# Optimization experiments

Hardware: AMD Instinct MI355X
Metric: run time of the kernel (lower is better)

The kernel has to match this reference:

```python
import jax, jax.numpy as jnp
import numpy as np

N, F, H = 512, 256, 512

def _w(k, i, o):
    return jax.random.normal(k, (i, o), jnp.float32) * (1.0 / np.sqrt(i))

def setup_inputs() -> dict:
    key = jax.random.key(0)
    ks = jax.random.split(key, 12)
    z = lambda n: jnp.zeros((n,), jnp.float32)
    return {
        "node_features": jax.random.normal(ks[0], (N, F), jnp.float32),
        "adjacency": jax.random.uniform(ks[1], (N, N), jnp.float32),
        # GraphConv layers: neighbor linear (wl,bl) and self-loop (ws,bs)
        "gc1_wl": _w(ks[2], F, H), "gc1_bl": z(H), "gc1_ws": _w(ks[3], F, H), "gc1_bs": z(H),
        "gc2_wl": _w(ks[4], H, H), "gc2_bl": z(H), "gc2_ws": _w(ks[5], H, H), "gc2_bs": z(H),
        "gc3_wl": _w(ks[6], H, F), "gc3_bl": z(F), "gc3_ws": _w(ks[7], H, F), "gc3_bs": z(F),
        # edge MLP: Linear(2F,H) -> ReLU -> (dropout=identity, eval) -> Linear(H,H) -> ReLU -> Linear(H,1)
        "mlp_w1": _w(ks[8], 2 * F, H), "mlp_b1": z(H),
        "mlp_w2": _w(ks[9], H, H), "mlp_b2": z(H),
        "mlp_w3": _w(ks[10], H, 1), "mlp_b3": z(1),
    }

def _gconv(x, adj_norm, wl, bl, ws, bs):
    # adj_norm @ Linear(x) + SelfLoop(x)
    return adj_norm @ (x @ wl + bl) + (x @ ws + bs)

def reference(node_features, adjacency,
              gc1_wl, gc1_bl, gc1_ws, gc1_bs,
              gc2_wl, gc2_bl, gc2_ws, gc2_bs,
              gc3_wl, gc3_bl, gc3_ws, gc3_bs,
              mlp_w1, mlp_b1, mlp_w2, mlp_b2, mlp_w3, mlp_b3):
    # row-normalized adjacency (shared across all three layers)
    adj_norm = adjacency / (adjacency.sum(axis=1, keepdims=True) + 1e-8)
    x = jax.nn.relu(_gconv(node_features, adj_norm, gc1_wl, gc1_bl, gc1_ws, gc1_bs))
    x = jax.nn.relu(_gconv(x, adj_norm, gc2_wl, gc2_bl, gc2_ws, gc2_bs))
    emb = _gconv(x, adj_norm, gc3_wl, gc3_bl, gc3_ws, gc3_bs)  # [N, F]
    # vectorized all-pairs (i<j) edge scoring, symmetric scatter
    iu, ju = np.triu_indices(N, k=1)  # static index lists, P = N(N-1)/2
    ef = jnp.concatenate([emb[iu], emb[ju]], axis=-1)  # [P, 2F]
    h = jax.nn.relu(ef @ mlp_w1 + mlp_b1)
    h = jax.nn.relu(h @ mlp_w2 + mlp_b2)
    s = jax.nn.sigmoid((h @ mlp_w3 + mlp_b3)[:, 0])  # [P]
    edge_scores = jnp.zeros((N, N), emb.dtype).at[iu, ju].set(s).at[ju, iu].set(s)
    return emb, edge_scores
```

## Files before the change

kernel.cpp:

```cpp
#include <hip/hip_runtime.h>
#include <hip/hip_bf16.h>


#define NN 512
#define FF 256
#define HH 512

typedef __attribute__((ext_vector_type(8))) short s8v;
typedef __attribute__((ext_vector_type(4))) float f4v;

__device__ __forceinline__ ushort f2bf(float f) {
  unsigned u = __float_as_uint(f);
  unsigned r = (u + 0x7fffu + ((u >> 16) & 1u)) >> 16;
  return (ushort)r;
}

__global__ __launch_bounds__(256)
void rownorm_kernel(const float* __restrict__ adj, float* __restrict__ adjn) {
  int row = blockIdx.x;
  int tid = threadIdx.x;
  const float* r = adj + row * NN;
  float a0 = r[tid], a1 = r[tid + 256];
  float s = a0 + a1;
#pragma unroll
  for (int m = 1; m < 64; m <<= 1) s += __shfl_xor(s, m);
  __shared__ float wsum[4];
  if ((tid & 63) == 0) wsum[tid >> 6] = s;
  __syncthreads();
  float inv = 1.f / (wsum[0] + wsum[1] + wsum[2] + wsum[3] + 1e-8f);
  float* o = adjn + row * NN;
  o[tid] = a0 * inv;
  o[tid + 256] = a1 * inv;
}

template <bool RELU>
__global__ __launch_bounds__(256)
void gemm_ts(int M, int N, int K,
             const float* __restrict__ A, int lda,
             const float* __restrict__ B0, const float* __restrict__ B1, int ldb,
             const float* __restrict__ bias0, const float* __restrict__ bias1,
             const float* __restrict__ add0, const float* __restrict__ add1, int ldadd,
             float* __restrict__ C0, float* __restrict__ C1, int ldc)
{
  const float* B = blockIdx.z ? B1 : B0;
  const float* bias = blockIdx.z ? bias1 : bias0;
  const float* add = blockIdx.z ? add1 : add0;
  float* C = blockIdx.z ? C1 : C0;
  const int n0 = blockIdx.x * 64;
  const int m0 = blockIdx.y * 16;
  const int tid = threadIdx.x;
  const int ty = tid >> 4, tx = tid & 15;

  __shared__ float As[32][18];
  __shared__ float Bs[32][68];
  float4 acc = {0.f, 0.f, 0.f, 0.f};

  const int am = tid >> 4;
  const int ak = tid & 15;
  const int bk = tid >> 4;
  const int bn = tid & 15;

  float2 pa = *(const float2*)&A[(m0 + am) * lda + ak * 2];
  float4 pb0 = *(const float4*)&B[bk * ldb + n0 + bn * 4];
  float4 pb1 = *(const float4*)&B[(bk + 16) * ldb + n0 + bn * 4];

  for (int k0 = 0; k0 < K; k0 += 32) {
    As[ak * 2][am] = pa.x;
    As[ak * 2 + 1][am] = pa.y;
    *(float4*)&Bs[bk][bn * 4] = pb0;
    *(float4*)&Bs[bk + 16][bn * 4] = pb1;
    __syncthreads();
    if (k0 + 32 < K) {
      pa = *(const float2*)&A[(m0 + am) * lda + k0 + 32 + ak * 2];
      pb0 = *(const float4*)&B[(k0 + 32 + bk) * ldb + n0 + bn * 4];
      pb1 = *(const float4*)&B[(k0 + 48 + bk) * ldb + n0 + bn * 4];
    }
#pragma unroll
    for (int k = 0; k < 32; ++k) {
      float a = As[k][ty];
      float4 b = *(const float4*)&Bs[k][tx * 4];
      acc.x += a * b.x; acc.y += a * b.y; acc.z += a * b.z; acc.w += a * b.w;
    }
    __syncthreads();
  }

  int m = m0 + ty;
  float4 v = acc;
  if (bias) {
    float4 bv = *(const float4*)&bias[n0 + tx * 4];
    v.x += bv.x; v.y += bv.y; v.z += bv.z; v.w += bv.w;
  }
  if (add) {
    float4 d = *(const float4*)&add[m * ldadd + n0 + tx * 4];
    v.x += d.x; v.y += d.y; v.z += d.z; v.w += d.w;
  }
  if (RELU) {
    v.x = fmaxf(v.x, 0.f); v.y = fmaxf(v.y, 0.f);
    v.z = fmaxf(v.z, 0.f); v.w = fmaxf(v.w, 0.f);
  }
  *(float4*)&C[m * ldc + n0 + tx * 4] = v;
}

__global__ __launch_bounds__(256)
void w2_pack(const float* __restrict__ w2, ushort* __restrict__ w2t2) {
  int slab = blockIdx.y;
  int col = blockIdx.x * 64 + (threadIdx.x >> 2);
  int kq = threadIdx.x & 3;
  int k0 = slab * 32 + kq * 8;
  ushort tmp[8];
#pragma unroll
  for (int e = 0; e < 8; ++e) tmp[e] = f2bf(w2[(k0 + e) * HH + col]);
  ushort* dst = w2t2 + slab * 16384 + col * 32 + kq * 8;
  *(ushort4*)dst = *(ushort4*)tmp;
  *(ushort4*)(dst + 4) = *(ushort4*)&tmp[4];
}

__global__ __launch_bounds__(512)
__attribute__((amdgpu_waves_per_eu(2, 2)))
void edge_mlp(const float* __restrict__ Amat, const float* __restrict__ Bmat,
              const ushort* __restrict__ w2t2,
              const float* __restrict__ b2, const float* __restrict__ w3,
              const float* __restrict__ b3,
              float* __restrict__ edges)
{
  __shared__ ushort h1s[2][128 * 128];
  __shared__ float part[8][640];

  const int tb = (int)blockIdx.x;
  int bj = (int)((sqrtf(4.f * tb + 1.f) - 1.f) * 0.5f);
  while (bj * bj + bj > tb) --bj;
  while ((bj + 1) * (bj + 2) <= tb) ++bj;
  const int bi = tb - bj * bj - bj;

  const int tid = threadIdx.x;
  const int wid = tid >> 6;
  const int lane = tid & 63;
  const int l15 = lane & 15;
  const int lg = lane >> 4;

  const f4v zero = {0.f, 0.f, 0.f, 0.f};
  f4v acc[8][4];
#pragma unroll
  for (int mf = 0; mf < 8; ++mf)
#pragma unroll
    for (int nf = 0; nf < 4; ++nf) acc[mf][nf] = zero;

  float4 sa[4], sb[4];
  auto issue_half = [&](int ch, int h) {
#pragma unroll
    for (int q = 0; q < 4; ++q) {
      int fidx = (h * 4 + q) * 512 + tid;
      int p = fidx >> 5;
      int k4 = fidx & 31;
      int i = bi * 8 + (p >> 4);
      int j = bj * 16 + (p & 15);
      sa[q] = *(const float4*)(Amat + i * HH + ch * 128 + k4 * 4);
      sb[q] = *(const float4*)(Bmat + j * HH + ch * 128 + k4 * 4);
    }
  };
  auto write_half = [&](int buf, int h) {
#pragma unroll
    for (int q = 0; q < 4; ++q) {
      int fidx = (h * 4 + q) * 512 + tid;
      int p = fidx >> 5;
      int k4 = fidx & 31;
      ushort4 pk;
      pk.x = f2bf(fmaxf(sa[q].x + sb[q].x, 0.f));
      pk.y = f2bf(fmaxf(sa[q].y + sb[q].y, 0.f));
      pk.z = f2bf(fmaxf(sa[q].z + sb[q].z, 0.f));
      pk.w = f2bf(fmaxf(sa[q].w + sb[q].w, 0.f));
      int off = (p * 256 + k4 * 8) ^ ((p & 7) << 4);
      *(ushort4*)((char*)h1s[buf] + off) = pk;
    }
  };

  issue_half(0, 0); write_half(0, 0);
  issue_half(0, 1); write_half(0, 1);
  __syncthreads();

  const ushort* wbase = w2t2 + wid * 2048 + l15 * 32 + lg * 8;

  s8v nb0, nb1, nb2, nb3;
  nb0 = *(const s8v*)wbase;
  nb1 = *(const s8v*)(wbase + 512);
  nb2 = *(const s8v*)(wbase + 1024);
  nb3 = *(const s8v*)(wbase + 1536);

  auto slab_step = [&](int cur, int slab) {
    s8v cb0 = nb0, cb1 = nb1, cb2 = nb2, cb3 = nb3;
    if (slab < 15) {
      const ushort* wb = wbase + (slab + 1) * 16384;
      nb0 = *(const s8v*)wb;
      nb1 = *(const s8v*)(wb + 512);
      nb2 = *(const s8v*)(wb + 1024);
      nb3 = *(const s8v*)(wb + 1536);
    }
    int ks = slab & 3;
#pragma unroll
    for (int mf = 0; mf < 8; ++mf) {
      int p = mf * 16 + l15;
      int off = (p * 256 + ks * 64 + lg * 16) ^ ((p & 7) << 4);
      s8v a = *(const s8v*)((const char*)h1s[cur] + off);
      acc[mf][0] = __builtin_amdgcn_mfma_f32_16x16x32_bf16(a, cb0, acc[mf][0], 0, 0, 0);
      acc[mf][1] = __builtin_amdgcn_mfma_f32_16x16x32_bf16(a, cb1, acc[mf][1], 0, 0, 0);
      acc[mf][2] = __builtin_amdgcn_mfma_f32_16x16x32_bf16(a, cb2, acc[mf][2], 0, 0, 0);
      acc[mf][3] = __builtin_amdgcn_mfma_f32_16x16x32_bf16(a, cb3, acc[mf][3], 0, 0, 0);
    }
  };

  for (int ch = 0; ch < 4; ++ch) {
    int cur = ch & 1;
    if (ch < 3) issue_half(ch + 1, 0);
    slab_step(cur, ch * 4 + 0);
    slab_step(cur, ch * 4 + 1);
    if (ch < 3) {
      write_half(cur ^ 1, 0);
      issue_half(ch + 1, 1);
    }
    slab_step(cur, ch * 4 + 2);
    slab_step(cur, ch * 4 + 3);
    if (ch < 3) write_half(cur ^ 1, 1);
    __syncthreads();
  }

  float bb[4], ww[4];
#pragma unroll
  for (int nf = 0; nf < 4; ++nf) {
    int col = wid * 64 + nf * 16 + l15;
    bb[nf] = b2[col];
    ww[nf] = w3[col];
  }
#pragma unroll
  for (int mf = 0; mf < 8; ++mf) {
    float ps[4];
#pragma unroll
    for (int e = 0; e < 4; ++e) {
      ps[e] = fmaxf(acc[mf][0][e] + bb[0], 0.f) * ww[0] +
              fmaxf(acc[mf][1][e] + bb[1], 0.f) * ww[1] +
              fmaxf(acc[mf][2][e] + bb[2], 0.f) * ww[2] +
              fmaxf(acc[mf][3][e] + bb[3], 0.f) * ww[3];
    }
#pragma unroll
    for (int m = 1; m < 16; m <<= 1) {
#pragma unroll
      for (int e = 0; e < 4; ++e) ps[e] += __shfl_xor(ps[e], m);
    }
    if (l15 == 0) {
#pragma unroll
      for (int e = 0; e < 4; ++e)
        part[wid][mf * 16 + lg * 4 + e] = ps[e];
    }
  }
  __syncthreads();
  if (tid < 128) {
    float tot = b3[0];
#pragma unroll
    for (int w = 0; w < 8; ++w) tot += part[w][tid];
    float sg = 1.f / (1.f + expf(-tot));
    int i = bi * 8 + (tid >> 4);
    int j = bj * 16 + (tid & 15);
    if (i < j) {
      edges[i * NN + j] = sg;
      edges[j * NN + i] = sg;
    } else if (i == j) {
      edges[i * NN + i] = 0.f;
    }
  }
}

extern "C" void kernel_launch(void* const* d_in, const int* in_sizes, int n_in,
                              void* d_out, int out_size, void* d_ws, size_t ws_size,
                              hipStream_t stream) {
  const float* node = (const float*)d_in[0];
  const float* adj  = (const float*)d_in[1];
  const float* g1wl = (const float*)d_in[2];
  const float* g1bl = (const float*)d_in[3];
  const float* g1ws = (const float*)d_in[4];
  const float* g1bs = (const float*)d_in[5];
  const float* g2wl = (const float*)d_in[6];
  const float* g2bl = (const float*)d_in[7];
  const float* g2ws = (const float*)d_in[8];
  const float* g2bs = (const float*)d_in[9];
  const float* g3wl = (const float*)d_in[10];
  const float* g3bl = (const float*)d_in[11];
  const float* g3ws = (const float*)d_in[12];
  const float* g3bs = (const float*)d_in[13];
  const float* w1 = (const float*)d_in[14];
  const float* b1 = (const float*)d_in[15];
  const float* w2 = (const float*)d_in[16];
  const float* b2 = (const float*)d_in[17];
  const float* w3 = (const float*)d_in[18];
  const float* b3 = (const float*)d_in[19];

  float* out = (float*)d_out;
  float* emb = out;
  float* edges = out + NN * FF;

  char* wsb = (char*)d_ws;
  float* adjn = (float*)wsb;
  float* Tb   = (float*)(wsb + (1u << 20));
  float* Sb   = (float*)(wsb + (2u << 20));
  float* xa   = (float*)(wsb + (3u << 20));
  float* xb   = (float*)(wsb + (4u << 20));
  ushort* w2t2 = (ushort*)(wsb + (5u << 20));
  float* Amat = Tb;
  float* Bmat = Sb;

  rownorm_kernel<<<NN, 256, 0, stream>>>(adj, adjn);
  w2_pack<<<dim3(8, 16), 256, 0, stream>>>(w2, w2t2);

  gemm_ts<false><<<dim3(8, 32, 2), 256, 0, stream>>>(
      NN, HH, FF, node, FF, g1wl, g1ws, HH, g1bl, g1bs,
      nullptr, nullptr, 0, Tb, Sb, HH);
  gemm_ts<true><<<dim3(8, 32, 1), 256, 0, stream>>>(
      NN, HH, NN, adjn, NN, Tb, Tb, HH, nullptr, nullptr,
      Sb, Sb, HH, xa, xa, HH);
  gemm_ts<false><<<dim3(8, 32, 2), 256, 0, stream>>>(
      NN, HH, HH, xa, HH, g2wl, g2ws, HH, g2bl, g2bs,
      nullptr, nullptr, 0, Tb, Sb, HH);
  gemm_ts<true><<<dim3(8, 32, 1), 256, 0, stream>>>(
      NN, HH, NN, adjn, NN, Tb, Tb, HH, nullptr, nullptr,
      Sb, Sb, HH, xb, xb, HH);
  gemm_ts<false><<<dim3(4, 32, 2), 256, 0, stream>>>(
      NN, FF, HH, xb, HH, g3wl, g3ws, FF, g3bl, g3bs,
      nullptr, nullptr, 0, Tb, Sb, FF);
  gemm_ts<false><<<dim3(4, 32, 1), 256, 0, stream>>>(
      NN, FF, NN, adjn, NN, Tb, Tb, FF, nullptr, nullptr,
      Sb, Sb, FF, emb, emb, FF);

  gemm_ts<false><<<dim3(8, 32, 2), 256, 0, stream>>>(
      NN, HH, FF, emb, FF, w1, w1 + FF * HH, HH, b1, nullptr,
      nullptr, nullptr, 0, Amat, Bmat, HH);

  edge_mlp<<<1056, 512, 0, stream>>>(Amat, Bmat, w2t2, b2, w3, b3, edges);
}
```

Baseline: 194.3 us.

## Merge prep kernels, halve GEMM row tile, raise MFMA wave priority

Folds the adjacency row-normalisation and the W2 bf16 packing into one launch, which removes a kernel launch. The small fp32 GEMMs drop from 16 to 8 rows per block, doubling the grid to fill more compute units, at the cost of less B-tile reuse per block. The edge MLP raises wave priority around its MFMA loop with s_setprio so matrix work is issued ahead of the other waves' loads.

```diff
diff --git a/kernel.cpp b/kernel.cpp
--- a/kernel.cpp
+++ b/kernel.cpp
@@ -16,103 +16,104 @@
 }
 
 __global__ __launch_bounds__(256)
-void rownorm_kernel(const float* __restrict__ adj, float* __restrict__ adjn) {
-  int row = blockIdx.x;
+void prep_kernel(const float* __restrict__ adj, float* __restrict__ adjn,
+                 const float* __restrict__ w2, ushort* __restrict__ w2t2) {
+  int b = blockIdx.x;
   int tid = threadIdx.x;
-  const float* r = adj + row * NN;
-  float a0 = r[tid], a1 = r[tid + 256];
-  float s = a0 + a1;
-#pragma unroll
-  for (int m = 1; m < 64; m <<= 1) s += __shfl_xor(s, m);
-  __shared__ float wsum[4];
-  if ((tid & 63) == 0) wsum[tid >> 6] = s;
-  __syncthreads();
-  float inv = 1.f / (wsum[0] + wsum[1] + wsum[2] + wsum[3] + 1e-8f);
-  float* o = adjn + row * NN;
-  o[tid] = a0 * inv;
-  o[tid + 256] = a1 * inv;
+  if (b < 512) {
+    const float* r = adj + b * NN;
+    float a0 = r[tid], a1 = r[tid + 256];
+    float s = a0 + a1;
+#pragma unroll
+    for (int m = 1; m < 64; m <<= 1) s += __shfl_xor(s, m);
+    __shared__ float wsum[4];
+    if ((tid & 63) == 0) wsum[tid >> 6] = s;
+    __syncthreads();
+    float inv = 1.f / (wsum[0] + wsum[1] + wsum[2] + wsum[3] + 1e-8f);
+    float* o = adjn + b * NN;
+    o[tid] = a0 * inv;
+    o[tid + 256] = a1 * inv;
+  } else {
+    int b2 = b - 512;
+    int slab = b2 >> 3;
+    int col = (b2 & 7) * 64 + (tid >> 2);
+    int kq = tid & 3;
+    int k0 = slab * 32 + kq * 8;
+    ushort tmp[8];
+#pragma unroll
+    for (int e = 0; e < 8; ++e) tmp[e] = f2bf(w2[(k0 + e) * HH + col]);
+    ushort* dst = w2t2 + slab * 16384 + col * 32 + kq * 8;
+    *(ushort4*)dst = *(ushort4*)tmp;
+    *(ushort4*)(dst + 4) = *(ushort4*)&tmp[4];
+  }
 }
 
 template <bool RELU>
 __global__ __launch_bounds__(256)
-void gemm_ts(int M, int N, int K,
-             const float* __restrict__ A, int lda,
-             const float* __restrict__ B0, const float* __restrict__ B1, int ldb,
-             const float* __restrict__ bias0, const float* __restrict__ bias1,
-             const float* __restrict__ add0, const float* __restrict__ add1, int ldadd,
-             float* __restrict__ C0, float* __restrict__ C1, int ldc)
+void gemm_ts8(int K,
+              const float* __restrict__ A, int lda,
+              const float* __restrict__ B0, const float* __restrict__ B1, int ldb,
+              const float* __restrict__ bias0, const float* __restrict__ bias1,
+              const float* __restrict__ add0, const float* __restrict__ add1, int ldadd,
+              float* __restrict__ C0, float* __restrict__ C1, int ldc)
 {
   const float* B = blockIdx.z ? B1 : B0;
   const float* bias = blockIdx.z ? bias1 : bias0;
   const float* add = blockIdx.z ? add1 : add0;
   float* C = blockIdx.z ? C1 : C0;
   const int n0 = blockIdx.x * 64;
-  const int m0 = blockIdx.y * 16;
+  const int m0 = blockIdx.y * 8;
   const int tid = threadIdx.x;
-  const int ty = tid >> 4, tx = tid & 15;
-
-  __shared__ float As[32][18];
-  __shared__ float Bs[32][68];
-  float4 acc = {0.f, 0.f, 0.f, 0.f};
-
-  const int am = tid >> 4;
-  const int ak = tid & 15;
-  const int bk = tid >> 4;
-  const int bn = tid & 15;
-
-  float2 pa = *(const float2*)&A[(m0 + am) * lda + ak * 2];
-  float4 pb0 = *(const float4*)&B[bk * ldb + n0 + bn * 4];
-  float4 pb1 = *(const float4*)&B[(bk + 16) * ldb + n0 + bn * 4];
+  const int row = tid >> 5;
+  const int cp = tid & 31;
+
+  __shared__ float As[32][9];
+  __shared__ float Bs[32][66];
+  float2 acc = {0.f, 0.f};
+
+  const int am = tid >> 5, ak = tid & 31;
+  const int br = tid >> 3, bc = (tid & 7) * 4;
+
+  float pa = A[(m0 + am) * lda + ak];
+  float4 pb0 = *(const float4*)&B[br * ldb + n0 + bc];
+  float4 pb1 = *(const float4*)&B[br * ldb + n0 + 32 + bc];
 
   for (int k0 = 0; k0 < K; k0 += 32) {
-    As[ak * 2][am] = pa.x;
-    As[ak * 2 + 1][am] = pa.y;
-    *(float4*)&Bs[bk][bn * 4] = pb0;
-    *(float4*)&Bs[bk + 16][bn * 4] = pb1;
+    As[ak][am] = pa;
+    *(float4*)&Bs[br][bc] = pb0;
+    *(float4*)&Bs[br][32 + bc] = pb1;
     __syncthreads();
     if (k0 + 32 < K) {
-      pa = *(const float2*)&A[(m0 + am) * lda + k0 + 32 + ak * 2];
-      pb0 = *(const float4*)&B[(k0 + 32 + bk) * ldb + n0 + bn * 4];
-      pb1 = *(const float4*)&B[(k0 + 48 + bk) * ldb + n0 + bn * 4];
+      pa = A[(m0 + am) * lda + k0 + 32 + ak];
+      pb0 = *(const float4*)&B[(k0 + 32 + br) * ldb + n0 + bc];
+      pb1 = *(const float4*)&B[(k0 + 32 + br) * ldb + n0 + 32 + bc];
     }
 #pragma unroll
     for (int k = 0; k < 32; ++k) {
-      float a = As[k][ty];
-      float4 b = *(const float4*)&Bs[k][tx * 4];
-      acc.x += a * b.x; acc.y += a * b.y; acc.z += a * b.z; acc.w += a * b.w;
+      float a = As[k][row];
+      float2 b = *(const float2*)&Bs[k][cp * 2];
+      acc.x += a * b.x;
+      acc.y += a * b.y;
     }
     __syncthreads();
   }
 
-  int m = m0 + ty;
-  float4 v = acc;
+  int m = m0 + row;
+  int col = n0 + cp * 2;
+  float2 v = acc;
   if (bias) {
-    float4 bv = *(const float4*)&bias[n0 + tx * 4];
-    v.x += bv.x; v.y += bv.y; v.z += bv.z; v.w += bv.w;
+    float2 bv = *(const float2*)&bias[col];
+    v.x += bv.x; v.y += bv.y;
   }
   if (add) {
-    float4 d = *(const float4*)&add[m * ldadd + n0 + tx * 4];
-    v.x += d.x; v.y += d.y; v.z += d.z; v.w += d.w;
+    float2 d = *(const float2*)&add[m * ldadd + col];
+    v.x += d.x; v.y += d.y;
   }
   if (RELU) {
-    v.x = fmaxf(v.x, 0.f); v.y = fmaxf(v.y, 0.f);
-    v.z = fmaxf(v.z, 0.f); v.w = fmaxf(v.w, 0.f);
-  }
-  *(float4*)&C[m * ldc + n0 + tx * 4] = v;
-}
-
-__global__ __launch_bounds__(256)
-void w2_pack(const float* __restrict__ w2, ushort* __restrict__ w2t2) {
-  int slab = blockIdx.y;
-  int col = blockIdx.x * 64 + (threadIdx.x >> 2);
-  int kq = threadIdx.x & 3;
-  int k0 = slab * 32 + kq * 8;
-  ushort tmp[8];
-#pragma unroll
-  for (int e = 0; e < 8; ++e) tmp[e] = f2bf(w2[(k0 + e) * HH + col]);
-  ushort* dst = w2t2 + slab * 16384 + col * 32 + kq * 8;
-  *(ushort4*)dst = *(ushort4*)tmp;
-  *(ushort4*)(dst + 4) = *(ushort4*)&tmp[4];
+    v.x = fmaxf(v.x, 0.f);
+    v.y = fmaxf(v.y, 0.f);
+  }
+  *(float2*)&C[m * ldc + col] = v;
 }
 
 __global__ __launch_bounds__(512)
@@ -196,6 +197,7 @@
       nb3 = *(const s8v*)(wb + 1536);
     }
     int ks = slab & 3;
+    __builtin_amdgcn_s_setprio(1);
 #pragma unroll
     for (int mf = 0; mf < 8; ++mf) {
       int p = mf * 16 + l15;
@@ -206,6 +208,7 @@
       acc[mf][2] = __builtin_amdgcn_mfma_f32_16x16x32_bf16(a, cb2, acc[mf][2], 0, 0, 0);
       acc[mf][3] = __builtin_amdgcn_mfma_f32_16x16x32_bf16(a, cb3, acc[mf][3], 0, 0, 0);
     }
+    __builtin_amdgcn_s_setprio(0);
   };
 
   for (int ch = 0; ch < 4; ++ch) {
@@ -306,30 +309,29 @@
   float* Amat = Tb;
   float* Bmat = Sb;
 
-  rownorm_kernel<<<NN, 256, 0, stream>>>(adj, adjn);
-  w2_pack<<<dim3(8, 16), 256, 0, stream>>>(w2, w2t2);
-
-  gemm_ts<false><<<dim3(8, 32, 2), 256, 0, stream>>>(
-      NN, HH, FF, node, FF, g1wl, g1ws, HH, g1bl, g1bs,
+  prep_kernel<<<640, 256, 0, stream>>>(adj, adjn, w2, w2t2);
+
+  gemm_ts8<false><<<dim3(8, 64, 2), 256, 0, stream>>>(
+      FF, node, FF, g1wl, g1ws, HH, g1bl, g1bs,
       nullptr, nullptr, 0, Tb, Sb, HH);
-  gemm_ts<true><<<dim3(8, 32, 1), 256, 0, stream>>>(
-      NN, HH, NN, adjn, NN, Tb, Tb, HH, nullptr, nullptr,
+  gemm_ts8<true><<<dim3(8, 64, 1), 256, 0, stream>>>(
+      NN, adjn, NN, Tb, Tb, HH, nullptr, nullptr,
       Sb, Sb, HH, xa, xa, HH);
-  gemm_ts<false><<<dim3(8, 32, 2), 256, 0, stream>>>(
-      NN, HH, HH, xa, HH, g2wl, g2ws, HH, g2bl, g2bs,
+  gemm_ts8<false><<<dim3(8, 64, 2), 256, 0, stream>>>(
+      HH, xa, HH, g2wl, g2ws, HH, g2bl, g2bs,
       nullptr, nullptr, 0, Tb, Sb, HH);
-  gemm_ts<true><<<dim3(8, 32, 1), 256, 0, stream>>>(
-      NN, HH, NN, adjn, NN, Tb, Tb, HH, nullptr, nullptr,
+  gemm_ts8<true><<<dim3(8, 64, 1), 256, 0, stream>>>(
+      NN, adjn, NN, Tb, Tb, HH, nullptr, nullptr,
       Sb, Sb, HH, xb, xb, HH);
-  gemm_ts<false><<<dim3(4, 32, 2), 256, 0, stream>>>(
-      NN, FF, HH, xb, HH, g3wl, g3ws, FF, g3bl, g3bs,
+  gemm_ts8<false><<<dim3(4, 64, 2), 256, 0, stream>>>(
+      HH, xb, HH, g3wl, g3ws, FF, g3bl, g3bs,
       nullptr, nullptr, 0, Tb, Sb, FF);
-  gemm_ts<false><<<dim3(4, 32, 1), 256, 0, stream>>>(
-      NN, FF, NN, adjn, NN, Tb, Tb, FF, nullptr, nullptr,
+  gemm_ts8<false><<<dim3(4, 64, 1), 256, 0, stream>>>(
+      NN, adjn, NN, Tb, Tb, FF, nullptr, nullptr,
       Sb, Sb, FF, emb, emb, FF);
 
-  gemm_ts<false><<<dim3(8, 32, 2), 256, 0, stream>>>(
-      NN, HH, FF, emb, FF, w1, w1 + FF * HH, HH, b1, nullptr,
+  gemm_ts8<false><<<dim3(8, 64, 2), 256, 0, stream>>>(
+      FF, emb, FF, w1, w1 + FF * HH, HH, b1, nullptr,
       nullptr, nullptr, 0, Amat, Bmat, HH);
 
   edge_mlp<<<1056, 512, 0, stream>>>(Amat, Bmat, w2t2, b2, w3, b3, edges);
```

Result: slower. 215.3 us (+10.8%).
